# Kernel optimization log

Measured on AMD Instinct MI355X. Metric: run time of the kernel, lower is better.

The kernel has to match this reference:

```python
import jax, jax.numpy as jnp
import numpy as np

B, S, D, H = 4, 2048, 1024, 16
HD = D // H  # head_dim = 64


def setup_inputs() -> dict:
    key = jax.random.key(0)
    ks = jax.random.split(key, 4)
    scale = 0.02
    return {
        "x": jax.random.normal(ks[0], (B, S, D), dtype=jnp.float32),
        "W_attn": jax.random.normal(ks[1], (D, 3 * D), dtype=jnp.float32) * scale,
        "b_attn": jnp.zeros((3 * D,), dtype=jnp.float32),
        "W_proj": jax.random.normal(ks[2], (D, D), dtype=jnp.float32) * scale,
        "b_proj": jnp.zeros((D,), dtype=jnp.float32),
    }


def reference(x, W_attn, b_attn, W_proj, b_proj):
    b, s, d = x.shape
    qkv = x @ W_attn + b_attn                      # [b, s, 3d]
    q, k, v = jnp.split(qkv, 3, axis=2)
    # [b, s, d] -> [b, h, s, hd]
    def to_heads(t):
        return t.reshape(b, s, H, HD).transpose(0, 2, 1, 3)
    q, k, v = to_heads(q), to_heads(k), to_heads(v)
    scores = jnp.einsum("bhqd,bhkd->bhqk", q, k) / jnp.sqrt(jnp.float32(HD))
    causal = jnp.tril(jnp.ones((s, s), dtype=bool))  # [s, s]
    scores = jnp.where(causal[None, None], scores, jnp.float32(-jnp.inf))
    probs = jax.nn.softmax(scores, axis=-1)
    y = jnp.einsum("bhqk,bhkd->bhqd", probs, v)    # [b, h, s, hd]
    y = y.transpose(0, 2, 1, 3).reshape(b, s, d)
    return y @ W_proj + b_proj
```

## Files before the change

kernel.cpp:

```cpp
#include <hip/hip_runtime.h>
#include <hip/hip_bf16.h>
#include <type_traits>

#define SQ    2048
#define DIM   1024
#define NH    16
#define HDIM  64
#define BATCH 4

typedef unsigned short u16;
typedef __bf16 bf16x8 __attribute__((ext_vector_type(8)));
typedef float  f32x4  __attribute__((ext_vector_type(4)));
typedef u16    u16x8  __attribute__((ext_vector_type(8)));

#define QSCALE 0.180336880f

__device__ __forceinline__ u16 f2bf(float f) {
  union { float f; unsigned u; } v; v.f = f;
  unsigned r = v.u + 0x7fffu + ((v.u >> 16) & 1u);
  return (u16)(r >> 16);
}

__device__ __forceinline__ float fast_exp2(float x) {
#if __has_builtin(__builtin_amdgcn_exp2f)
  return __builtin_amdgcn_exp2f(x);
#else
  float y;
  asm("v_exp_f32 %0, %1" : "=v"(y) : "v"(x));
  return y;
#endif
}

__device__ __forceinline__ void gll16(const u16* g, u16* l) {
  __builtin_amdgcn_global_load_lds((const __attribute__((address_space(1))) void*)g,
                                   (__attribute__((address_space(3))) void*)l,
                                   16, 0, 0);
}

__global__ __launch_bounds__(256)
void f32_to_bf16_vec(const float* __restrict__ in, u16* __restrict__ out, int n4)
{
  const int i = blockIdx.x * blockDim.x + threadIdx.x;
  if (i < n4) {
    const float4 v = ((const float4*)in)[i];
    ushort4 o;
    o.x = f2bf(v.x); o.y = f2bf(v.y); o.z = f2bf(v.z); o.w = f2bf(v.w);
    ((ushort4*)out)[i] = o;
  }
}

__global__ void transpose_f32_bf16(const float* __restrict__ in, u16* __restrict__ out,
                                   int R, int C)
{
  __shared__ u16 tile[32][33];
  const int bx = blockIdx.x * 32, by = blockIdx.y * 32;
  const int tx = threadIdx.x, ty = threadIdx.y;
  #pragma unroll
  for (int i = 0; i < 32; i += 8)
    tile[ty + i][tx] = f2bf(in[(size_t)(by + ty + i) * C + bx + tx]);
  __syncthreads();
  #pragma unroll
  for (int i = 0; i < 32; i += 8)
    out[(size_t)(bx + ty + i) * R + by + tx] = tile[tx][ty + i];
}

template<int MODE>
__global__ __launch_bounds__(256)
void gemm_bt(const u16* __restrict__ A, const u16* __restrict__ Bt,
             const float* __restrict__ bias, int K,
             u16* __restrict__ o0, u16* __restrict__ o1, float* __restrict__ of)
{
  __shared__ __align__(16) u16 A0[128 * 32], A1[128 * 32];
  __shared__ __align__(16) u16 B0[128 * 32], B1[128 * 32];

  const int t    = threadIdx.x;
  const int lane = t & 63, wave = t >> 6;
  const int l15  = lane & 15, quad = lane >> 4;
  const int wm   = (wave & 1) * 64, wn = (wave >> 1) * 64;
  const int m0   = blockIdx.y * 128, n0 = blockIdx.x * 128;

  const int srow = wave * 32 + (lane >> 2);
  const int scol = (lane & 3) * 8;

  f32x4 acc[4][4] = {};

  for (int k0 = 0; k0 < K; k0 += 64) {
    const u16* ga = A  + (size_t)(m0 + srow) * K + k0 + scol;
    const u16* gb = Bt + (size_t)(n0 + srow) * K + k0 + scol;
    gll16(ga,              &A0[(wave * 32)      * 32]);
    gll16(ga + 32,         &A1[(wave * 32)      * 32]);
    gll16(ga + 16 * K,     &A0[(wave * 32 + 16) * 32]);
    gll16(ga + 16 * K + 32,&A1[(wave * 32 + 16) * 32]);
    gll16(gb,              &B0[(wave * 32)      * 32]);
    gll16(gb + 32,         &B1[(wave * 32)      * 32]);
    gll16(gb + 16 * K,     &B0[(wave * 32 + 16) * 32]);
    gll16(gb + 16 * K + 32,&B1[(wave * 32 + 16) * 32]);
    __syncthreads();

    #pragma unroll
    for (int ks = 0; ks < 2; ++ks) {
      const u16* Als = ks ? A1 : A0;
      const u16* Bls = ks ? B1 : B0;
      bf16x8 af[4], bfr[4];
      #pragma unroll
      for (int i = 0; i < 4; ++i) af[i]  = *(const bf16x8*)&Als[(wm + 16*i + l15) * 32 + quad * 8];
      #pragma unroll
      for (int j = 0; j < 4; ++j) bfr[j] = *(const bf16x8*)&Bls[(wn + 16*j + l15) * 32 + quad * 8];
      #pragma unroll
      for (int i = 0; i < 4; ++i)
        #pragma unroll
        for (int j = 0; j < 4; ++j)
          acc[i][j] = (MODE == 2)
            ? __builtin_amdgcn_mfma_f32_16x16x32_bf16(bfr[j], af[i], acc[i][j], 0, 0, 0)
            : __builtin_amdgcn_mfma_f32_16x16x32_bf16(af[i], bfr[j], acc[i][j], 0, 0, 0);
    }
    __syncthreads();
  }

  if (MODE == 2) {
    #pragma unroll
    for (int j = 0; j < 4; ++j) {
      #pragma unroll
      for (int r = 0; r < 4; ++r) {
        const int d = n0 + wn + 16*j + quad * 4 + r;
        const float bn = bias[d];
        const int h = d >> 6, hd = d & 63;
        #pragma unroll
        for (int i = 0; i < 4; ++i) {
          const int m = m0 + wm + 16*i + l15;
          const int b = m >> 11, s = m & 2047;
          o0[(((size_t)(b * NH + h)) * HDIM + hd) * SQ + s] = f2bf(acc[i][j][r] + bn);
        }
      }
    }
  } else {
    #pragma unroll
    for (int j = 0; j < 4; ++j) {
      const int n = n0 + wn + 16*j + l15;
      const float bn = bias[n];
      #pragma unroll
      for (int i = 0; i < 4; ++i) {
        #pragma unroll
        for (int r = 0; r < 4; ++r) {
          const int m = m0 + wm + 16*i + quad * 4 + r;
          const float val = acc[i][j][r] + bn;
          if (MODE == 1) {
            const int sec = n >> 10, d = n & 1023;
            const int h = d >> 6, hd = d & 63;
            const int b = m >> 11, s = m & 2047;
            const int bh = b * NH + h;
            if (sec == 0) o0[((size_t)bh * SQ + s) * HDIM + hd] = f2bf(val * QSCALE);
            else          o1[((size_t)bh * SQ + s) * HDIM + hd] = f2bf(val);
          } else {
            of[(size_t)m * DIM + n] = val;
          }
        }
      }
    }
  }
}

__global__ __launch_bounds__(256, 2)
void attn_fused(const u16* __restrict__ q_ws, const u16* __restrict__ k_ws,
                const u16* __restrict__ v_t, u16* __restrict__ y_ws)
{
  __shared__ __align__(16) u16 Kls[2][64 * 64];
  __shared__ __align__(16) u16 Vls[2][64 * 64];
  __shared__ __align__(16) u16 Pls[4][64 * 64];

  const int bh = blockIdx.x;
  const int p  = blockIdx.y;
  const int b = bh >> 4, h = bh & 15;
  const int t = threadIdx.x;
  const int lane = t & 63, wave = t >> 6;
  const int l15 = lane & 15, quad = lane >> 4;
  const int rx  = l15 & 7;
  const int cK0 = ((quad      ^ rx) << 3);
  const int cK1 = (((quad | 4) ^ rx) << 3);
  const int pswz = rx << 3;

  const u16* Q  = q_ws + (size_t)bh * SQ * HDIM;
  const u16* Kp = k_ws + (size_t)bh * SQ * HDIM;
  const u16* Vp = v_t  + (size_t)bh * HDIM * SQ;

  const int qtH = 15 - p, qtL = p;
  const int qrowH = qtH * 128 + wave * 32;
  const int qrowL = qtL * 128 + wave * 32;

  bf16x8 qf[4][2];
  #pragma unroll
  for (int s = 0; s < 4; ++s) {
    const int qrow = ((s < 2) ? qrowH : qrowL) + 16 * (s & 1);
    #pragma unroll
    for (int ks = 0; ks < 2; ++ks)
      qf[s][ks] = *(const bf16x8*)&Q[(size_t)(qrow + l15) * HDIM + ks * 32 + quad * 8];
  }

  f32x4 o[4][4] = {};
  float l_q[4] = {};

  const int r3   = lane >> 3;
  const int c8   = lane & 7;
  const int scol = ((c8 ^ r3) << 3);

  auto stage = [&](int kv0, int buf) {
    gll16(&Kp[(size_t)(kv0 + wave*16     + r3) * HDIM + scol], &Kls[buf][(wave*16    ) * 64]);
    gll16(&Kp[(size_t)(kv0 + wave*16 + 8 + r3) * HDIM + scol], &Kls[buf][(wave*16 + 8) * 64]);
    gll16(&Vp[(size_t)(wave*16     + r3) * SQ + kv0 + scol],   &Vls[buf][(wave*16    ) * 64]);
    gll16(&Vp[(size_t)(wave*16 + 8 + r3) * SQ + kv0 + scol],   &Vls[buf][(wave*16 + 8) * 64]);
  };

  auto compute = [&](int kv0, int buf, auto doLc, auto mHc, auto mLc) {
    constexpr bool DO_L = decltype(doLc)::value;
    constexpr bool MH   = decltype(mHc)::value;
    constexpr bool ML   = decltype(mLc)::value;
    constexpr int  NS   = DO_L ? 4 : 2;
    f32x4 st[4][4] = {};
    const u16* Kb = Kls[buf];
    __builtin_amdgcn_s_setprio(1);
    #pragma unroll
    for (int ks = 0; ks < 2; ++ks) {
      const int cs = ks ? cK1 : cK0;
      #pragma unroll
      for (int kt = 0; kt < 4; ++kt) {
        bf16x8 kf = *(const bf16x8*)&Kb[(16*kt + l15) * 64 + cs];
        #pragma unroll
        for (int s = 0; s < NS; ++s)
          st[s][kt] = __builtin_amdgcn_mfma_f32_16x16x32_bf16(kf, qf[s][ks], st[s][kt], 0, 0, 0);
      }
    }
    __builtin_amdgcn_s_setprio(0);

    #pragma unroll
    for (int s = 0; s < NS; ++s) {
      const bool msk = (s < 2) ? MH : ML;
      const int qrow = ((s < 2) ? qrowH : qrowL) + 16 * (s & 1);
      const int q = qrow + l15;
      float rsum = 0.f;
      #pragma unroll
      for (int kt = 0; kt < 4; ++kt)
        #pragma unroll
        for (int r = 0; r < 4; ++r) {
          float pv = fast_exp2(st[s][kt][r]);
          if (msk && (kv0 + 16*kt + quad*4 + r) > q) pv = 0.f;
          st[s][kt][r] = pv;
          rsum += pv;
        }
      l_q[s] += rsum;
    }

    #pragma unroll
    for (int s = 0; s < NS; ++s)
      #pragma unroll
      for (int kt = 0; kt < 4; ++kt) {
        union { __hip_bfloat162 h2[2]; ushort4 u4; } pk;
        pk.h2[0] = __float22bfloat162_rn(make_float2(st[s][kt][0], st[s][kt][1]));
        pk.h2[1] = __float22bfloat162_rn(make_float2(st[s][kt][2], st[s][kt][3]));
        *(ushort4*)&Pls[wave][(16*s + l15) * 64 + ((16*kt + quad*4) ^ pswz)] = pk.u4;
      }

    const u16* Vb = Vls[buf];
    __builtin_amdgcn_s_setprio(1);
    #pragma unroll
    for (int ks = 0; ks < 2; ++ks) {
      const int cs = ks ? cK1 : cK0;
      bf16x8 vf[4];
      #pragma unroll
      for (int n = 0; n < 4; ++n)
        vf[n] = *(const bf16x8*)&Vb[(16*n + l15) * 64 + cs];
      #pragma unroll
      for (int s = 0; s < NS; ++s) {
        bf16x8 pa = *(const bf16x8*)&Pls[wave][(16*s + l15) * 64 + ((ks*32 + quad*8) ^ pswz)];
        #pragma unroll
        for (int n = 0; n < 4; ++n)
          o[s][n] = __builtin_amdgcn_mfma_f32_16x16x32_bf16(pa, vf[n], o[s][n], 0, 0, 0);
      }
    }
    __builtin_amdgcn_s_setprio(0);
  };

  const int ntiles = 2 * qtH + 2;
  const int lastH  = 2 * qtH + (wave >> 1);
  const int lastL  = 2 * qtL + (wave >> 1);

  using Fc = std::integral_constant<bool, false>;
  using Tc = std::integral_constant<bool, true>;

  stage(0, 0);
  for (int kvt = 0; kvt < ntiles; ++kvt) {
    const int cur = kvt & 1;
    const int kv0 = kvt * 64;
    __syncthreads();
    if (kvt + 1 < ntiles) stage((kvt + 1) * 64, cur ^ 1);
    if      (kvt <  lastL) compute(kv0, cur, Tc{}, Fc{}, Fc{});
    else if (kvt == lastL) compute(kv0, cur, Tc{}, Fc{}, Tc{});
    else if (kvt <  lastH) compute(kv0, cur, Fc{}, Fc{}, Fc{});
    else if (kvt == lastH) compute(kv0, cur, Fc{}, Tc{}, Fc{});
  }

  #pragma unroll
  for (int s = 0; s < 4; ++s) {
    l_q[s] += __shfl_xor(l_q[s], 16);
    l_q[s] += __shfl_xor(l_q[s], 32);
  }
  #pragma unroll
  for (int s = 0; s < 4; ++s) {
    const int qrow = ((s < 2) ? qrowH : qrowL) + 16 * (s & 1);
    #pragma unroll
    for (int r = 0; r < 4; ++r) {
      const float lr = __shfl(l_q[s], quad * 4 + r);
      const float inv = 1.0f / lr;
      const int qg = qrow + quad * 4 + r;
      #pragma unroll
      for (int n = 0; n < 4; ++n)
        y_ws[((size_t)b * SQ + qg) * DIM + h * HDIM + 16*n + l15] = f2bf(o[s][n][r] * inv);
    }
  }
}

extern "C" void kernel_launch(void* const* d_in, const int* in_sizes, int n_in,
                              void* d_out, int out_size, void* d_ws, size_t ws_size,
                              hipStream_t stream)
{
  const float* x      = (const float*)d_in[0];
  const float* W_attn = (const float*)d_in[1];
  const float* b_attn = (const float*)d_in[2];
  const float* W_proj = (const float*)d_in[3];
  const float* b_proj = (const float*)d_in[4];
  float* out = (float*)d_out;

  char* ws = (char*)d_ws;
  u16* WattnT = (u16*)(ws);
  u16* WprojT = (u16*)(ws + 6291456);
  u16* xb     = (u16*)(ws + 8388608);
  u16* y_ws   = xb;
  u16* q_ws   = (u16*)(ws + 25165824);
  u16* k_ws   = (u16*)(ws + 41943040);
  u16* v_tw   = (u16*)(ws + 58720256);

  const dim3 tb(32, 8);
  transpose_f32_bf16<<<dim3(3 * DIM / 32, DIM / 32), tb, 0, stream>>>(W_attn, WattnT, DIM, 3 * DIM);
  transpose_f32_bf16<<<dim3(DIM / 32, DIM / 32), tb, 0, stream>>>(W_proj, WprojT, DIM, DIM);
  f32_to_bf16_vec<<<(BATCH * SQ * DIM / 4 + 255) / 256, 256, 0, stream>>>(x, xb, BATCH * SQ * DIM / 4);

  gemm_bt<1><<<dim3(2 * DIM / 128, BATCH * SQ / 128), 256, 0, stream>>>(
      xb, WattnT, b_attn, DIM, q_ws, k_ws, nullptr);
  gemm_bt<2><<<dim3(DIM / 128, BATCH * SQ / 128), 256, 0, stream>>>(
      xb, WattnT + (size_t)2048 * DIM, b_attn + 2048, DIM, v_tw, nullptr, nullptr);

  attn_fused<<<dim3(BATCH * NH, 8), 256, 0, stream>>>(q_ws, k_ws, v_tw, y_ws);

  gemm_bt<0><<<dim3(DIM / 128, BATCH * SQ / 128), 256, 0, stream>>>(
      y_ws, WprojT, b_proj, DIM, nullptr, nullptr, out);
}
```

Measured before the change: 256.1 us.

## Add 256x256-tile 8-wave GEMM kernel for the Q/K projection

Adds a new gemm256 kernel with 256x256 output tiles, 512 threads, double-buffered LDS loaded through direct global-to-LDS loads, and loads interleaved between four MFMA phases using barriers and setprio. Only the Q/K projection GEMM switches to it; the V projection and output projection keep the old 128-tile kernel. Larger tiles raise arithmetic intensity and cut global traffic per FLOP. In exchange the kernel needs 128 KB of LDS and many accumulator registers, which limits occupancy, and the grid shrinks to 256 blocks.

```diff
diff --git a/kernel.cpp b/kernel.cpp
--- a/kernel.cpp
+++ b/kernel.cpp
@@ -160,6 +160,176 @@
   }
 }
 
+template<int MODE>
+__global__ __launch_bounds__(512)
+void gemm256(const u16* __restrict__ A, const u16* __restrict__ Bt,
+             const float* __restrict__ bias, int K,
+             u16* __restrict__ o0, u16* __restrict__ o1, float* __restrict__ of)
+{
+  __shared__ __align__(16) u16 Als[2][256 * 64];
+  __shared__ __align__(16) u16 Bls[2][256 * 64];
+
+  const int t    = threadIdx.x;
+  const int lane = t & 63, wave = t >> 6;
+  const int l15  = lane & 15, quad = lane >> 4;
+  const int wm   = (wave >> 2) * 128;
+  const int wn   = (wave & 3) * 64;
+  const int m0   = blockIdx.y * 256, n0 = blockIdx.x * 256;
+
+  const int rx  = l15 & 7;
+  const int cS0 = ((quad       ^ rx) << 3);
+  const int cS1 = (((quad | 4) ^ rx) << 3);
+
+  const int r3 = lane >> 3, c8 = lane & 7;
+  const int scol = ((c8 ^ r3) << 3);
+
+  const u16* gA = A  + (size_t)(m0 + wave * 8 + r3) * K + scol;
+  const u16* gB = Bt + (size_t)(n0 + wave * 8 + r3) * K + scol;
+  const size_t pstride = (size_t)64 * K;
+
+  f32x4 acc[8][4] = {};
+
+  auto stA = [&](int k0, int buf, int p) {
+    gll16(gA + (size_t)p * pstride + k0, &Als[buf][(p * 64 + wave * 8) * 64]);
+  };
+  auto stB = [&](int k0, int buf, int p) {
+    gll16(gB + (size_t)p * pstride + k0, &Bls[buf][(p * 64 + wave * 8) * 64]);
+  };
+
+  stA(0, 0, 0); stA(0, 0, 2); stB(0, 0, 0); stB(0, 0, 1);
+  stB(0, 0, 2); stB(0, 0, 3); stA(0, 0, 1); stA(0, 0, 3);
+  asm volatile("s_waitcnt vmcnt(2)" ::: "memory");
+  __builtin_amdgcn_s_barrier();
+  __builtin_amdgcn_sched_barrier(0);
+
+  const int NT = K >> 6;
+  for (int tt = 0; tt < NT; ++tt) {
+    const int cur = tt & 1, nxt = cur ^ 1;
+    const int k1  = (tt + 1) << 6;
+    const bool st = (tt + 1 < NT);
+    const u16* Ab = &Als[cur][0];
+    const u16* Bb = &Bls[cur][0];
+    bf16x8 af[4], bf0[4], bf1[4];
+
+    #pragma unroll
+    for (int nj = 0; nj < 4; ++nj)
+      bf0[nj] = *(const bf16x8*)&Bb[(wn + 16 * nj + l15) * 64 + cS0];
+    #pragma unroll
+    for (int mi = 0; mi < 4; ++mi)
+      af[mi] = *(const bf16x8*)&Ab[(wm + 16 * mi + l15) * 64 + cS0];
+    if (st) { stA(k1, nxt, 0); stA(k1, nxt, 2); }
+    __builtin_amdgcn_s_barrier();
+    __builtin_amdgcn_s_setprio(1);
+    #pragma unroll
+    for (int mi = 0; mi < 4; ++mi)
+      #pragma unroll
+      for (int nj = 0; nj < 4; ++nj)
+        acc[mi][nj] = (MODE == 2)
+          ? __builtin_amdgcn_mfma_f32_16x16x32_bf16(bf0[nj], af[mi], acc[mi][nj], 0, 0, 0)
+          : __builtin_amdgcn_mfma_f32_16x16x32_bf16(af[mi], bf0[nj], acc[mi][nj], 0, 0, 0);
+    __builtin_amdgcn_s_setprio(0);
+    if (st) asm volatile("s_waitcnt vmcnt(2)" ::: "memory");
+    else    asm volatile("s_waitcnt vmcnt(0)" ::: "memory");
+    __builtin_amdgcn_s_barrier();
+    __builtin_amdgcn_sched_barrier(0);
+
+    #pragma unroll
+    for (int mi = 0; mi < 4; ++mi)
+      af[mi] = *(const bf16x8*)&Ab[(wm + 64 + 16 * mi + l15) * 64 + cS0];
+    if (st) { stB(k1, nxt, 0); stB(k1, nxt, 1); }
+    __builtin_amdgcn_s_barrier();
+    __builtin_amdgcn_s_setprio(1);
+    #pragma unroll
+    for (int mi = 0; mi < 4; ++mi)
+      #pragma unroll
+      for (int nj = 0; nj < 4; ++nj)
+        acc[4 + mi][nj] = (MODE == 2)
+          ? __builtin_amdgcn_mfma_f32_16x16x32_bf16(bf0[nj], af[mi], acc[4 + mi][nj], 0, 0, 0)
+          : __builtin_amdgcn_mfma_f32_16x16x32_bf16(af[mi], bf0[nj], acc[4 + mi][nj], 0, 0, 0);
+    __builtin_amdgcn_s_setprio(0);
+    __builtin_amdgcn_s_barrier();
+
+    #pragma unroll
+    for (int nj = 0; nj < 4; ++nj)
+      bf1[nj] = *(const bf16x8*)&Bb[(wn + 16 * nj + l15) * 64 + cS1];
+    #pragma unroll
+    for (int mi = 0; mi < 4; ++mi)
+      af[mi] = *(const bf16x8*)&Ab[(wm + 16 * mi + l15) * 64 + cS1];
+    if (st) { stB(k1, nxt, 2); stB(k1, nxt, 3); }
+    __builtin_amdgcn_s_barrier();
+    __builtin_amdgcn_s_setprio(1);
+    #pragma unroll
+    for (int mi = 0; mi < 4; ++mi)
+      #pragma unroll
+      for (int nj = 0; nj < 4; ++nj)
+        acc[mi][nj] = (MODE == 2)
+          ? __builtin_amdgcn_mfma_f32_16x16x32_bf16(bf1[nj], af[mi], acc[mi][nj], 0, 0, 0)
+          : __builtin_amdgcn_mfma_f32_16x16x32_bf16(af[mi], bf1[nj], acc[mi][nj], 0, 0, 0);
+    __builtin_amdgcn_s_setprio(0);
+    __builtin_amdgcn_s_barrier();
+
+    #pragma unroll
+    for (int mi = 0; mi < 4; ++mi)
+      af[mi] = *(const bf16x8*)&Ab[(wm + 64 + 16 * mi + l15) * 64 + cS1];
+    if (st) { stA(k1, nxt, 1); stA(k1, nxt, 3); }
+    __builtin_amdgcn_s_barrier();
+    __builtin_amdgcn_s_setprio(1);
+    #pragma unroll
+    for (int mi = 0; mi < 4; ++mi)
+      #pragma unroll
+      for (int nj = 0; nj < 4; ++nj)
+        acc[4 + mi][nj] = (MODE == 2)
+          ? __builtin_amdgcn_mfma_f32_16x16x32_bf16(bf1[nj], af[mi], acc[4 + mi][nj], 0, 0, 0)
+          : __builtin_amdgcn_mfma_f32_16x16x32_bf16(af[mi], bf1[nj], acc[4 + mi][nj], 0, 0, 0);
+    __builtin_amdgcn_s_setprio(0);
+    if (st) asm volatile("s_waitcnt vmcnt(2)" ::: "memory");
+    __builtin_amdgcn_s_barrier();
+    __builtin_amdgcn_sched_barrier(0);
+  }
+
+  if (MODE == 2) {
+    #pragma unroll
+    for (int j = 0; j < 4; ++j) {
+      #pragma unroll
+      for (int r = 0; r < 4; ++r) {
+        const int d = n0 + wn + 16 * j + quad * 4 + r;
+        const float bn = bias[d];
+        const int h = d >> 6, hd = d & 63;
+        #pragma unroll
+        for (int i = 0; i < 8; ++i) {
+          const int m = m0 + wm + 16 * i + l15;
+          const int b = m >> 11, s = m & 2047;
+          o0[(((size_t)(b * NH + h)) * HDIM + hd) * SQ + s] = f2bf(acc[i][j][r] + bn);
+        }
+      }
+    }
+  } else {
+    #pragma unroll
+    for (int j = 0; j < 4; ++j) {
+      const int n = n0 + wn + 16 * j + l15;
+      const float bn = bias[n];
+      #pragma unroll
+      for (int i = 0; i < 8; ++i) {
+        #pragma unroll
+        for (int r = 0; r < 4; ++r) {
+          const int m = m0 + wm + 16 * i + quad * 4 + r;
+          const float val = acc[i][j][r] + bn;
+          if (MODE == 1) {
+            const int sec = n >> 10, d = n & 1023;
+            const int h = d >> 6, hd = d & 63;
+            const int b = m >> 11, s = m & 2047;
+            const int bh = b * NH + h;
+            if (sec == 0) o0[((size_t)bh * SQ + s) * HDIM + hd] = f2bf(val * QSCALE);
+            else          o1[((size_t)bh * SQ + s) * HDIM + hd] = f2bf(val);
+          } else {
+            of[(size_t)m * DIM + n] = val;
+          }
+        }
+      }
+    }
+  }
+}
+
 __global__ __launch_bounds__(256, 2)
 void attn_fused(const u16* __restrict__ q_ws, const u16* __restrict__ k_ws,
                 const u16* __restrict__ v_t, u16* __restrict__ y_ws)
@@ -343,7 +513,7 @@
   transpose_f32_bf16<<<dim3(DIM / 32, DIM / 32), tb, 0, stream>>>(W_proj, WprojT, DIM, DIM);
   f32_to_bf16_vec<<<(BATCH * SQ * DIM / 4 + 255) / 256, 256, 0, stream>>>(x, xb, BATCH * SQ * DIM / 4);
 
-  gemm_bt<1><<<dim3(2 * DIM / 128, BATCH * SQ / 128), 256, 0, stream>>>(
+  gemm256<1><<<dim3(2 * DIM / 256, BATCH * SQ / 256), 512, 0, stream>>>(
       xb, WattnT, b_attn, DIM, q_ws, k_ws, nullptr);
   gemm_bt<2><<<dim3(DIM / 128, BATCH * SQ / 128), 256, 0, stream>>>(
       xb, WattnT + (size_t)2048 * DIM, b_attn + 2048, DIM, v_tw, nullptr, nullptr);
```

Result: faster. 249.8 us (-2.5%).
